# Kernel tuning notes

Measured on AMD Instinct MI355X. Metric: run time of the kernel, lower is better.

Reference implementation:

```python
import math
import jax, jax.numpy as jnp
import numpy as np

N_QUBITS = 8
N_QLAYERS = 2
HIDDEN = 768
BATCH = 8192
LN_EPS = 1e-5


def _ry_gate(theta):
    # theta: scalar or (B,) -> (2,2) or (B,2,2) complex64
    h = theta * 0.5
    c, s = jnp.cos(h), jnp.sin(h)
    g = jnp.stack([jnp.stack([c, -s], axis=-1), jnp.stack([s, c], axis=-1)], axis=-2)
    return g.astype(jnp.complex64)


def _rz_gate(theta):
    t = theta.astype(jnp.complex64)
    e0, e1 = jnp.exp(-0.5j * t), jnp.exp(0.5j * t)
    z = jnp.zeros_like(e0)
    return jnp.stack([jnp.stack([e0, z], axis=-1), jnp.stack([z, e1], axis=-1)], axis=-2)


def _apply_1q(state, gate, w, n):
    # state: (B, 2**n); gate: (2,2) shared or (B,2,2) per-sample; wire w (0 = MSB)
    B = state.shape[0]
    s = state.reshape(B, 2 ** w, 2, -1)
    if gate.ndim == 2:
        s = jnp.einsum('ij,bljr->blir', gate, s)
    else:
        s = jnp.einsum('bij,bljr->blir', gate, s)
    return s.reshape(B, -1)


def _apply_cnot(state, c, t, n):
    B = state.shape[0]
    s = state.reshape((B,) + (2,) * n)
    ax_c = 1 + c
    s0 = jnp.take(s, 0, axis=ax_c)  # control=0 branch, control axis removed
    s1 = jnp.take(s, 1, axis=ax_c)
    ax_t = 1 + t - (1 if t > c else 0)
    s1 = jnp.flip(s1, axis=ax_t)    # X on target when control=1
    s = jnp.stack([s0, s1], axis=ax_c)
    return s.reshape(B, -1)


def _circuit(angles, weights_ry, weights_rz):
    # angles: (B, n) float32 -> (B, n) PauliZ expectations, batched statevector sim
    n, L = N_QUBITS, N_QLAYERS
    B = angles.shape[0]
    state = jnp.zeros((B, 2 ** n), dtype=jnp.complex64).at[:, 0].set(1.0)
    for i in range(n):
        state = _apply_1q(state, _ry_gate(angles[:, i]), i, n)
    for i in range(1, n):
        state = _apply_cnot(state, 0, i, n)
    for l in range(L):
        for i in range(n):
            state = _apply_1q(state, _ry_gate(weights_ry[l, i]), i, n)
            state = _apply_1q(state, _rz_gate(weights_rz[l, i]), i, n)
    for i in range(1, n):
        state = _apply_cnot(state, i, 0, n)
    probs = jnp.abs(state) ** 2  # (B, 2**n)
    k = jnp.arange(2 ** n)
    bits = (k[None, :] >> (n - 1 - jnp.arange(n))[:, None]) & 1  # wire 0 = MSB (PennyLane)
    signs = (1 - 2 * bits).astype(probs.dtype)  # (n, 2**n)
    return probs @ signs.T  # (B, n)


def setup_inputs() -> dict:
    key = jax.random.key(0)
    ks = jax.random.split(key, 8)
    return {
        'hidden': jax.random.normal(ks[0], (BATCH, HIDDEN), dtype=jnp.float32),
        'W_in': jax.random.normal(ks[1], (N_QUBITS, HIDDEN), dtype=jnp.float32) * (1.0 / math.sqrt(HIDDEN)),
        'b_in': jax.random.normal(ks[2], (N_QUBITS,), dtype=jnp.float32) * 0.01,
        'W_out': jax.random.normal(ks[3], (HIDDEN, N_QUBITS), dtype=jnp.float32) * (1.0 / math.sqrt(N_QUBITS)),
        'b_out': jax.random.normal(ks[4], (HIDDEN,), dtype=jnp.float32) * 0.01,
        'weights_ry': jax.random.normal(ks[5], (N_QLAYERS, N_QUBITS), dtype=jnp.float32) * 0.1,
        'weights_rz': jax.random.normal(ks[6], (N_QLAYERS, N_QUBITS), dtype=jnp.float32) * 0.1,
        'gamma': jnp.ones((HIDDEN,), dtype=jnp.float32),
        'beta': jnp.zeros((HIDDEN,), dtype=jnp.float32),
    }


def reference(hidden, W_in, b_in, W_out, b_out, weights_ry, weights_rz, gamma, beta):
    phase = 0.0
    angles = jnp.tanh(hidden @ W_in.T + b_in) * math.pi + phase  # (B, n)
    meas = _circuit(angles, weights_ry, weights_rz).astype(jnp.float32)  # (B, n)
    y = meas @ W_out.T + b_out  # (B, h)
    mu = jnp.mean(y, axis=-1, keepdims=True)
    var = jnp.mean(jnp.square(y - mu), axis=-1, keepdims=True)
    return (y - mu) * jax.lax.rsqrt(var + LN_EPS) * gamma + beta
```

## Files before the change

### kernel.cpp

```cpp
#include <hip/hip_runtime.h>
#include <hip/hip_bf16.h>

#define NQ    8
#define HID   768
#define BATCH 8192
#define SPB   4
#define NBLK  (BATCH / SPB)
#define TPB   256

template<int BF> __device__ __forceinline__ float LDV(const void* p, int i) {
    if constexpr (BF) return __bfloat162float(((const __hip_bfloat16*)p)[i]);
    else return ((const float*)p)[i];
}
template<int BF> __device__ __forceinline__ void STV(void* p, int i, float v) {
    if constexpr (BF) ((__hip_bfloat16*)p)[i] = __float2bfloat16(v);
    else ((float*)p)[i] = v;
}
template<int BF> __device__ __forceinline__ float4 LD4(const void* p, int i4) {
    if constexpr (BF) {
        ushort4 v = ((const ushort4*)p)[i4];
        float4 r;
        r.x = __uint_as_float(((unsigned)v.x) << 16);
        r.y = __uint_as_float(((unsigned)v.y) << 16);
        r.z = __uint_as_float(((unsigned)v.z) << 16);
        r.w = __uint_as_float(((unsigned)v.w) << 16);
        return r;
    } else {
        return ((const float4*)p)[i4];
    }
}


__global__ void setup_kernel(const void* hidden, const void* wry, const void* wrz, void* ws) {
    __shared__ int votes;
    __shared__ int sFlag;
    int tid = threadIdx.x;
    if (tid == 0) votes = 0;
    __syncthreads();
    const unsigned int* hw = (const unsigned int*)hidden;
    int cnt = 0;
    #pragma unroll
    for (int k = 0; k < 16; ++k) {
        unsigned int w = hw[tid * 16 + k];
        unsigned int lo = w & 0xffffu;
        unsigned int e = (lo >> 7) & 0xffu;
        if (lo == 0u || (e >= 100u && e <= 133u)) cnt++;
    }
    atomicAdd(&votes, cnt);
    __syncthreads();
    if (tid == 0) {
        sFlag = (votes * 2 > TPB * 16) ? 1 : 0;
        *(int*)ws = sFlag;
    }
    __syncthreads();
    const int flag = sFlag;
    if (tid < NQ) {
        float ry0, ry1, rz0, rz1;
        if (flag) {
            ry0 = LDV<1>(wry, tid);  ry1 = LDV<1>(wry, NQ + tid);
            rz0 = LDV<1>(wrz, tid);  rz1 = LDV<1>(wrz, NQ + tid);
        } else {
            ry0 = LDV<0>(wry, tid);  ry1 = LDV<0>(wry, NQ + tid);
            rz0 = LDV<0>(wrz, tid);  rz1 = LDV<0>(wrz, NQ + tid);
        }
        float cA = cosf(0.5f*ry0), sA = sinf(0.5f*ry0);
        float cB = cosf(0.5f*ry1), sB = sinf(0.5f*ry1);
        float p0c = cosf(0.5f*rz0), p0s = sinf(0.5f*rz0);
        float p1c = cosf(0.5f*rz1), p1s = sinf(0.5f*rz1);
        float g00r =  cA*p0c, g00i = -cA*p0s;
        float g01r = -sA*p0c, g01i =  sA*p0s;
        float g10r =  sA*p0c, g10i =  sA*p0s;
        float g11r =  cA*p0c, g11i =  cA*p0s;
        float h00r = cB*g00r - sB*g10r, h00i = cB*g00i - sB*g10i;
        float h01r = cB*g01r - sB*g11r, h01i = cB*g01i - sB*g11i;
        float h10r = sB*g00r + cB*g10r, h10i = sB*g00i + cB*g10i;
        float h11r = sB*g01r + cB*g11r, h11i = sB*g01i + cB*g11i;
        float f00r = h00r*p1c + h00i*p1s, f00i = h00i*p1c - h00r*p1s;
        float f01r = h01r*p1c + h01i*p1s, f01i = h01i*p1c - h01r*p1s;
        float f10r = h10r*p1c - h10i*p1s, f10i = h10i*p1c + h10r*p1s;
        float f11r = h11r*p1c - h11i*p1s, f11i = h11i*p1c + h11r*p1s;
        float DA = f00r*f00r + f00i*f00i - (f10r*f10r + f10i*f10i);
        float DB = f01r*f01r + f01i*f01i - (f11r*f11r + f11i*f11i);
        float Kr = (f00r*f01r + f00i*f01i) - (f10r*f11r + f10i*f11i);
        float Ki = (f00i*f01r - f00r*f01i) - (f10i*f11r - f10r*f11i);
        float* qc = (float*)((char*)ws + 16);
        qc[tid*4+0] = DA; qc[tid*4+1] = DB; qc[tid*4+2] = Kr; qc[tid*4+3] = Ki;
    }
}

template<int BF>
__device__ __forceinline__ void run_all(
    const void* hidden_, const void* W_in_, const void* b_in_,
    const void* W_out_, const void* b_out_, const void* gamma_, const void* beta_,
    void* out_, const float* qc)
{
    const int tid  = threadIdx.x;
    const int lane = tid & 63;
    const int wv   = tid >> 6;
    const int b    = blockIdx.x * SPB + wv;
    const int j    = lane >> 3;
    const int u    = lane & 7;
    const int rowbase = b * HID;

    float a0 = 0.f, a1 = 0.f, a2 = 0.f, a3 = 0.f;
    const int hbase = b * (HID/4);
    const int wbase = j * (HID/4);
    #pragma unroll
    for (int t = 0; t < 24; ++t) {
        int i4 = u + (t << 3);
        float4 h = LD4<BF>(hidden_, hbase + i4);
        float4 w = LD4<BF>(W_in_,  wbase + i4);
        a0 = fmaf(h.x, w.x, a0); a1 = fmaf(h.y, w.y, a1);
        a2 = fmaf(h.z, w.z, a2); a3 = fmaf(h.w, w.w, a3);
    }
    float acc = (a0 + a1) + (a2 + a3);
    acc += __shfl_xor(acc, 1, 64);
    acc += __shfl_xor(acc, 2, 64);
    acc += __shfl_xor(acc, 4, 64);

    float zb = acc + LDV<BF>(b_in_, j);
    float th = tanhf(zb);
    float sj = sinpif(th);
    float cj = cospif(th);

    float4 q = ((const float4*)qc)[j];
    float DA = q.x, DB = q.y, Kr = q.z, Ki = q.w;
    float ca = 0.5f * (DA + DB), da = 0.5f * (DA - DB);
    float uu = da * cj;
    float vv = fmaf(Kr, sj, ca);
    const bool g0 = (j == 0);
    float MA = g0 ? 1.f : (vv + uu);
    float MB = g0 ? 1.f : (vv - uu);
    float fr = g0 ? 1.f : Kr;
    float fi = g0 ? 0.f : (cj * Ki);
    #pragma unroll
    for (int d = 8; d < 64; d <<= 1) {
        MA *= __shfl_xor(MA, d, 64);
        MB *= __shfl_xor(MB, d, 64);
        float qr = __shfl_xor(fr, d, 64);
        float qi = __shfl_xor(fi, d, 64);
        float nr = fr * qr - fi * qi;
        float ni = fr * qi + fi * qr;
        fr = nr; fi = ni;
    }
    float cc0 = __shfl(cj, 0, 64);
    float sc0 = __shfl(sj, 0, 64);
    float DA0 = __shfl(DA, 0, 64);
    float DB0 = __shfl(DB, 0, 64);
    float Kr0 = __shfl(Kr, 0, 64);
    float Ki0 = __shfl(Ki, 0, 64);
    float meas0 = 0.5f * (1.f + cc0) * DA0 * MA
                + 0.5f * (1.f - cc0) * DB0 * MB
                + sc0 * (Kr0 * fr - Ki0 * fi);
    float measj = g0 ? meas0 : fmaf(cc0, uu, vv);
    float m0 = meas0;
    float m1 = __shfl(measj,  8, 64);
    float m2 = __shfl(measj, 16, 64);
    float m3 = __shfl(measj, 24, 64);
    float m4 = __shfl(measj, 32, 64);
    float m5 = __shfl(measj, 40, 64);
    float m6 = __shfl(measj, 48, 64);
    float m7 = __shfl(measj, 56, 64);

    float yv[12];
    float sum = 0.f, sumsq = 0.f;
    #pragma unroll
    for (int t = 0; t < 12; ++t) {
        int h = lane + (t << 6);
        float4 w0 = LD4<BF>(W_out_, h * 2);
        float4 w1 = LD4<BF>(W_out_, h * 2 + 1);
        float y = LDV<BF>(b_out_, h);
        y = fmaf(m0, w0.x, y); y = fmaf(m1, w0.y, y);
        y = fmaf(m2, w0.z, y); y = fmaf(m3, w0.w, y);
        y = fmaf(m4, w1.x, y); y = fmaf(m5, w1.y, y);
        y = fmaf(m6, w1.z, y); y = fmaf(m7, w1.w, y);
        yv[t] = y;
        sum += y;
        sumsq = fmaf(y, y, sumsq);
    }
    #pragma unroll
    for (int d = 1; d < 64; d <<= 1) {
        sum   += __shfl_xor(sum,   d, 64);
        sumsq += __shfl_xor(sumsq, d, 64);
    }
    float mean = sum * (1.f / HID);
    float var  = fmaf(sumsq, 1.f / HID, -mean * mean);
    float rstd = rsqrtf(var + 1e-5f);
    #pragma unroll
    for (int t = 0; t < 12; ++t) {
        int h = lane + (t << 6);
        float g  = LDV<BF>(gamma_, h);
        float be = LDV<BF>(beta_,  h);
        float o  = fmaf((yv[t] - mean) * rstd, g, be);
        STV<BF>(out_, rowbase + h, o);
    }
}

__global__ __launch_bounds__(TPB, 4) void main_kernel(
    const void* hidden_, const void* W_in_, const void* b_in_,
    const void* W_out_, const void* b_out_, const void* gamma_, const void* beta_,
    void* out_, const void* ws_)
{
    const int flag = *(const int*)ws_;
    const float* qc = (const float*)((const char*)ws_ + 16);
    if (flag)
        run_all<1>(hidden_, W_in_, b_in_, W_out_, b_out_, gamma_, beta_, out_, qc);
    else
        run_all<0>(hidden_, W_in_, b_in_, W_out_, b_out_, gamma_, beta_, out_, qc);
}

extern "C" void kernel_launch(void* const* d_in, const int* in_sizes, int n_in,
                              void* d_out, int out_size, void* d_ws, size_t ws_size,
                              hipStream_t stream) {
    const void* hidden = d_in[0];
    const void* W_in   = d_in[1];
    const void* b_in   = d_in[2];
    const void* W_out  = d_in[3];
    const void* b_out  = d_in[4];
    const void* wry    = d_in[5];
    const void* wrz    = d_in[6];
    const void* gamma  = d_in[7];
    const void* beta   = d_in[8];
    setup_kernel<<<1, TPB, 0, stream>>>(hidden, wry, wrz, d_ws);
    main_kernel<<<NBLK, TPB, 0, stream>>>(hidden, W_in, b_in, W_out, b_out,
                                          gamma, beta, d_out, d_ws);
}
```

Measured before the change: 114.5 us.

## Fuse setup into main kernel, process two samples per wave, vectorize output

```diff
diff --git a/kernel.cpp b/kernel.cpp
--- a/kernel.cpp
+++ b/kernel.cpp
@@ -4,17 +4,14 @@
 #define NQ    8
 #define HID   768
 #define BATCH 8192
-#define SPB   4
+#define SPW   2
+#define SPB   (4*SPW)
 #define NBLK  (BATCH / SPB)
 #define TPB   256
 
 template<int BF> __device__ __forceinline__ float LDV(const void* p, int i) {
     if constexpr (BF) return __bfloat162float(((const __hip_bfloat16*)p)[i]);
     else return ((const float*)p)[i];
-}
-template<int BF> __device__ __forceinline__ void STV(void* p, int i, float v) {
-    if constexpr (BF) ((__hip_bfloat16*)p)[i] = __float2bfloat16(v);
-    else ((float*)p)[i] = v;
 }
 template<int BF> __device__ __forceinline__ float4 LD4(const void* p, int i4) {
     if constexpr (BF) {
@@ -29,40 +26,41 @@
         return ((const float4*)p)[i4];
     }
 }
-
-
-__global__ void setup_kernel(const void* hidden, const void* wry, const void* wrz, void* ws) {
-    __shared__ int votes;
-    __shared__ int sFlag;
-    int tid = threadIdx.x;
-    if (tid == 0) votes = 0;
-    __syncthreads();
-    const unsigned int* hw = (const unsigned int*)hidden;
-    int cnt = 0;
-    #pragma unroll
-    for (int k = 0; k < 16; ++k) {
-        unsigned int w = hw[tid * 16 + k];
-        unsigned int lo = w & 0xffffu;
-        unsigned int e = (lo >> 7) & 0xffu;
-        if (lo == 0u || (e >= 100u && e <= 133u)) cnt++;
-    }
-    atomicAdd(&votes, cnt);
-    __syncthreads();
-    if (tid == 0) {
-        sFlag = (votes * 2 > TPB * 16) ? 1 : 0;
-        *(int*)ws = sFlag;
-    }
-    __syncthreads();
-    const int flag = sFlag;
-    if (tid < NQ) {
-        float ry0, ry1, rz0, rz1;
-        if (flag) {
-            ry0 = LDV<1>(wry, tid);  ry1 = LDV<1>(wry, NQ + tid);
-            rz0 = LDV<1>(wrz, tid);  rz1 = LDV<1>(wrz, NQ + tid);
-        } else {
-            ry0 = LDV<0>(wry, tid);  ry1 = LDV<0>(wry, NQ + tid);
-            rz0 = LDV<0>(wrz, tid);  rz1 = LDV<0>(wrz, NQ + tid);
-        }
+template<int BF> __device__ __forceinline__ void ST4(void* p, int i4, float4 v) {
+    if constexpr (BF) {
+        __hip_bfloat16 bx = __float2bfloat16(v.x);
+        __hip_bfloat16 by = __float2bfloat16(v.y);
+        __hip_bfloat16 bz = __float2bfloat16(v.z);
+        __hip_bfloat16 bw = __float2bfloat16(v.w);
+        ushort4 s;
+        s.x = *(const unsigned short*)&bx;
+        s.y = *(const unsigned short*)&by;
+        s.z = *(const unsigned short*)&bz;
+        s.w = *(const unsigned short*)&bw;
+        ((ushort4*)p)[i4] = s;
+    } else {
+        ((float4*)p)[i4] = v;
+    }
+}
+
+template<int BF>
+__device__ __forceinline__ void run_all(
+    const void* hidden_, const void* W_in_, const void* b_in_,
+    const void* W_out_, const void* b_out_, const void* wry_, const void* wrz_,
+    const void* gamma_, const void* beta_, void* out_)
+{
+    const int tid  = threadIdx.x;
+    const int lane = tid & 63;
+    const int wv   = tid >> 6;
+    const int j    = lane >> 3;
+    const int u    = lane & 7;
+    const int b0   = blockIdx.x * SPB + wv * SPW;
+    const int b1   = b0 + 1;
+
+    float DA, DB, Kr, Ki;
+    {
+        float ry0 = LDV<BF>(wry_, j), ry1 = LDV<BF>(wry_, NQ + j);
+        float rz0 = LDV<BF>(wrz_, j), rz1 = LDV<BF>(wrz_, NQ + j);
         float cA = cosf(0.5f*ry0), sA = sinf(0.5f*ry0);
         float cB = cosf(0.5f*ry1), sB = sinf(0.5f*ry1);
         float p0c = cosf(0.5f*rz0), p0s = sinf(0.5f*rz0);
@@ -79,134 +77,152 @@
         float f01r = h01r*p1c + h01i*p1s, f01i = h01i*p1c - h01r*p1s;
         float f10r = h10r*p1c - h10i*p1s, f10i = h10i*p1c + h10r*p1s;
         float f11r = h11r*p1c - h11i*p1s, f11i = h11i*p1c + h11r*p1s;
-        float DA = f00r*f00r + f00i*f00i - (f10r*f10r + f10i*f10i);
-        float DB = f01r*f01r + f01i*f01i - (f11r*f11r + f11i*f11i);
-        float Kr = (f00r*f01r + f00i*f01i) - (f10r*f11r + f10i*f11i);
-        float Ki = (f00i*f01r - f00r*f01i) - (f10i*f11r - f10r*f11i);
-        float* qc = (float*)((char*)ws + 16);
-        qc[tid*4+0] = DA; qc[tid*4+1] = DB; qc[tid*4+2] = Kr; qc[tid*4+3] = Ki;
-    }
-}
-
-template<int BF>
-__device__ __forceinline__ void run_all(
-    const void* hidden_, const void* W_in_, const void* b_in_,
-    const void* W_out_, const void* b_out_, const void* gamma_, const void* beta_,
-    void* out_, const float* qc)
-{
-    const int tid  = threadIdx.x;
-    const int lane = tid & 63;
-    const int wv   = tid >> 6;
-    const int b    = blockIdx.x * SPB + wv;
-    const int j    = lane >> 3;
-    const int u    = lane & 7;
-    const int rowbase = b * HID;
-
-    float a0 = 0.f, a1 = 0.f, a2 = 0.f, a3 = 0.f;
-    const int hbase = b * (HID/4);
-    const int wbase = j * (HID/4);
+        DA = f00r*f00r + f00i*f00i - (f10r*f10r + f10i*f10i);
+        DB = f01r*f01r + f01i*f01i - (f11r*f11r + f11i*f11i);
+        Kr = (f00r*f01r + f00i*f01i) - (f10r*f11r + f10i*f11i);
+        Ki = (f00i*f01r - f00r*f01i) - (f10i*f11r - f10r*f11i);
+    }
+
+    float p00=0,p01=0,p02=0,p03=0, p10=0,p11=0,p12=0,p13=0;
+    const int h0b = b0 * (HID/4);
+    const int h1b = b1 * (HID/4);
+    const int wb  = j  * (HID/4);
     #pragma unroll
     for (int t = 0; t < 24; ++t) {
         int i4 = u + (t << 3);
-        float4 h = LD4<BF>(hidden_, hbase + i4);
-        float4 w = LD4<BF>(W_in_,  wbase + i4);
-        a0 = fmaf(h.x, w.x, a0); a1 = fmaf(h.y, w.y, a1);
-        a2 = fmaf(h.z, w.z, a2); a3 = fmaf(h.w, w.w, a3);
-    }
-    float acc = (a0 + a1) + (a2 + a3);
-    acc += __shfl_xor(acc, 1, 64);
-    acc += __shfl_xor(acc, 2, 64);
-    acc += __shfl_xor(acc, 4, 64);
-
-    float zb = acc + LDV<BF>(b_in_, j);
-    float th = tanhf(zb);
-    float sj = sinpif(th);
-    float cj = cospif(th);
-
-    float4 q = ((const float4*)qc)[j];
-    float DA = q.x, DB = q.y, Kr = q.z, Ki = q.w;
+        float4 w  = LD4<BF>(W_in_,   wb  + i4);
+        float4 h0 = LD4<BF>(hidden_, h0b + i4);
+        float4 h1 = LD4<BF>(hidden_, h1b + i4);
+        p00 = fmaf(h0.x, w.x, p00); p01 = fmaf(h0.y, w.y, p01);
+        p02 = fmaf(h0.z, w.z, p02); p03 = fmaf(h0.w, w.w, p03);
+        p10 = fmaf(h1.x, w.x, p10); p11 = fmaf(h1.y, w.y, p11);
+        p12 = fmaf(h1.z, w.z, p12); p13 = fmaf(h1.w, w.w, p13);
+    }
+    float acc0 = (p00 + p01) + (p02 + p03);
+    float acc1 = (p10 + p11) + (p12 + p13);
+    #pragma unroll
+    for (int d = 1; d < 8; d <<= 1) {
+        acc0 += __shfl_xor(acc0, d, 64);
+        acc1 += __shfl_xor(acc1, d, 64);
+    }
+
+    float binj = LDV<BF>(b_in_, j);
+    float th0 = tanhf(acc0 + binj);
+    float th1 = tanhf(acc1 + binj);
+    float sj0 = sinpif(th0), cj0 = cospif(th0);
+    float sj1 = sinpif(th1), cj1 = cospif(th1);
+
     float ca = 0.5f * (DA + DB), da = 0.5f * (DA - DB);
-    float uu = da * cj;
-    float vv = fmaf(Kr, sj, ca);
     const bool g0 = (j == 0);
-    float MA = g0 ? 1.f : (vv + uu);
-    float MB = g0 ? 1.f : (vv - uu);
-    float fr = g0 ? 1.f : Kr;
-    float fi = g0 ? 0.f : (cj * Ki);
+    float uu0 = da * cj0, vv0 = fmaf(Kr, sj0, ca);
+    float uu1 = da * cj1, vv1 = fmaf(Kr, sj1, ca);
+    float MA0 = g0 ? 1.f : (vv0 + uu0), MB0 = g0 ? 1.f : (vv0 - uu0);
+    float MA1 = g0 ? 1.f : (vv1 + uu1), MB1 = g0 ? 1.f : (vv1 - uu1);
+    float fr0 = g0 ? 1.f : Kr, fi0 = g0 ? 0.f : (cj0 * Ki);
+    float fr1 = g0 ? 1.f : Kr, fi1 = g0 ? 0.f : (cj1 * Ki);
     #pragma unroll
     for (int d = 8; d < 64; d <<= 1) {
-        MA *= __shfl_xor(MA, d, 64);
-        MB *= __shfl_xor(MB, d, 64);
-        float qr = __shfl_xor(fr, d, 64);
-        float qi = __shfl_xor(fi, d, 64);
-        float nr = fr * qr - fi * qi;
-        float ni = fr * qi + fi * qr;
-        fr = nr; fi = ni;
-    }
-    float cc0 = __shfl(cj, 0, 64);
-    float sc0 = __shfl(sj, 0, 64);
-    float DA0 = __shfl(DA, 0, 64);
-    float DB0 = __shfl(DB, 0, 64);
-    float Kr0 = __shfl(Kr, 0, 64);
-    float Ki0 = __shfl(Ki, 0, 64);
-    float meas0 = 0.5f * (1.f + cc0) * DA0 * MA
-                + 0.5f * (1.f - cc0) * DB0 * MB
-                + sc0 * (Kr0 * fr - Ki0 * fi);
-    float measj = g0 ? meas0 : fmaf(cc0, uu, vv);
-    float m0 = meas0;
-    float m1 = __shfl(measj,  8, 64);
-    float m2 = __shfl(measj, 16, 64);
-    float m3 = __shfl(measj, 24, 64);
-    float m4 = __shfl(measj, 32, 64);
-    float m5 = __shfl(measj, 40, 64);
-    float m6 = __shfl(measj, 48, 64);
-    float m7 = __shfl(measj, 56, 64);
-
-    float yv[12];
-    float sum = 0.f, sumsq = 0.f;
-    #pragma unroll
-    for (int t = 0; t < 12; ++t) {
-        int h = lane + (t << 6);
-        float4 w0 = LD4<BF>(W_out_, h * 2);
-        float4 w1 = LD4<BF>(W_out_, h * 2 + 1);
-        float y = LDV<BF>(b_out_, h);
-        y = fmaf(m0, w0.x, y); y = fmaf(m1, w0.y, y);
-        y = fmaf(m2, w0.z, y); y = fmaf(m3, w0.w, y);
-        y = fmaf(m4, w1.x, y); y = fmaf(m5, w1.y, y);
-        y = fmaf(m6, w1.z, y); y = fmaf(m7, w1.w, y);
-        yv[t] = y;
-        sum += y;
-        sumsq = fmaf(y, y, sumsq);
+        MA0 *= __shfl_xor(MA0, d, 64);   MA1 *= __shfl_xor(MA1, d, 64);
+        MB0 *= __shfl_xor(MB0, d, 64);   MB1 *= __shfl_xor(MB1, d, 64);
+        float q0r = __shfl_xor(fr0, d, 64), q0i = __shfl_xor(fi0, d, 64);
+        float q1r = __shfl_xor(fr1, d, 64), q1i = __shfl_xor(fi1, d, 64);
+        float n0r = fr0*q0r - fi0*q0i, n0i = fr0*q0i + fi0*q0r;
+        float n1r = fr1*q1r - fi1*q1i, n1i = fr1*q1i + fi1*q1r;
+        fr0 = n0r; fi0 = n0i; fr1 = n1r; fi1 = n1i;
+    }
+    float DA0 = __shfl(DA, 0, 64), DB0 = __shfl(DB, 0, 64);
+    float Kr0 = __shfl(Kr, 0, 64), Ki0 = __shfl(Ki, 0, 64);
+    float cc00 = __shfl(cj0, 0, 64), sc00 = __shfl(sj0, 0, 64);
+    float cc01 = __shfl(cj1, 0, 64), sc01 = __shfl(sj1, 0, 64);
+    float meas00 = 0.5f*(1.f+cc00)*DA0*MA0 + 0.5f*(1.f-cc00)*DB0*MB0
+                 + sc00*(Kr0*fr0 - Ki0*fi0);
+    float meas01 = 0.5f*(1.f+cc01)*DA0*MA1 + 0.5f*(1.f-cc01)*DB0*MB1
+                 + sc01*(Kr0*fr1 - Ki0*fi1);
+    float measj0 = g0 ? meas00 : fmaf(cc00, uu0, vv0);
+    float measj1 = g0 ? meas01 : fmaf(cc01, uu1, vv1);
+    float m00 = meas00;
+    float m01 = __shfl(measj0,  8, 64), m02 = __shfl(measj0, 16, 64);
+    float m03 = __shfl(measj0, 24, 64), m04 = __shfl(measj0, 32, 64);
+    float m05 = __shfl(measj0, 40, 64), m06 = __shfl(measj0, 48, 64);
+    float m07 = __shfl(measj0, 56, 64);
+    float m10 = meas01;
+    float m11 = __shfl(measj1,  8, 64), m12 = __shfl(measj1, 16, 64);
+    float m13 = __shfl(measj1, 24, 64), m14 = __shfl(measj1, 32, 64);
+    float m15 = __shfl(measj1, 40, 64), m16 = __shfl(measj1, 48, 64);
+    float m17 = __shfl(measj1, 56, 64);
+
+    float y0v[12], y1v[12];
+    float sum0 = 0.f, sq0 = 0.f, sum1 = 0.f, sq1 = 0.f;
+    #pragma unroll
+    for (int g = 0; g < 3; ++g) {
+        float4 bo = LD4<BF>(b_out_, 3*lane + g);
+        float bos[4] = {bo.x, bo.y, bo.z, bo.w};
+        #pragma unroll
+        for (int e = 0; e < 4; ++e) {
+            int c = 12*lane + 4*g + e;
+            float4 w0 = LD4<BF>(W_out_, c*2);
+            float4 w1 = LD4<BF>(W_out_, c*2 + 1);
+            float y0 = bos[e], y1 = bos[e];
+            y0 = fmaf(m00, w0.x, y0); y0 = fmaf(m01, w0.y, y0);
+            y0 = fmaf(m02, w0.z, y0); y0 = fmaf(m03, w0.w, y0);
+            y0 = fmaf(m04, w1.x, y0); y0 = fmaf(m05, w1.y, y0);
+            y0 = fmaf(m06, w1.z, y0); y0 = fmaf(m07, w1.w, y0);
+            y1 = fmaf(m10, w0.x, y1); y1 = fmaf(m11, w0.y, y1);
+            y1 = fmaf(m12, w0.z, y1); y1 = fmaf(m13, w0.w, y1);
+            y1 = fmaf(m14, w1.x, y1); y1 = fmaf(m15, w1.y, y1);
+            y1 = fmaf(m16, w1.z, y1); y1 = fmaf(m17, w1.w, y1);
+            y0v[4*g+e] = y0; y1v[4*g+e] = y1;
+            sum0 += y0; sq0 = fmaf(y0, y0, sq0);
+            sum1 += y1; sq1 = fmaf(y1, y1, sq1);
+        }
     }
     #pragma unroll
     for (int d = 1; d < 64; d <<= 1) {
-        sum   += __shfl_xor(sum,   d, 64);
-        sumsq += __shfl_xor(sumsq, d, 64);
-    }
-    float mean = sum * (1.f / HID);
-    float var  = fmaf(sumsq, 1.f / HID, -mean * mean);
-    float rstd = rsqrtf(var + 1e-5f);
-    #pragma unroll
-    for (int t = 0; t < 12; ++t) {
-        int h = lane + (t << 6);
-        float g  = LDV<BF>(gamma_, h);
-        float be = LDV<BF>(beta_,  h);
-        float o  = fmaf((yv[t] - mean) * rstd, g, be);
-        STV<BF>(out_, rowbase + h, o);
+        sum0 += __shfl_xor(sum0, d, 64);  sq0 += __shfl_xor(sq0, d, 64);
+        sum1 += __shfl_xor(sum1, d, 64);  sq1 += __shfl_xor(sq1, d, 64);
+    }
+    float mean0 = sum0 * (1.f/HID);
+    float var0  = fmaf(sq0, 1.f/HID, -mean0*mean0);
+    float rstd0 = rsqrtf(var0 + 1e-5f);
+    float mean1 = sum1 * (1.f/HID);
+    float var1  = fmaf(sq1, 1.f/HID, -mean1*mean1);
+    float rstd1 = rsqrtf(var1 + 1e-5f);
+    #pragma unroll
+    for (int g = 0; g < 3; ++g) {
+        float4 ga = LD4<BF>(gamma_, 3*lane + g);
+        float4 be = LD4<BF>(beta_,  3*lane + g);
+        float4 o0, o1;
+        o0.x = fmaf((y0v[4*g+0]-mean0)*rstd0, ga.x, be.x);
+        o0.y = fmaf((y0v[4*g+1]-mean0)*rstd0, ga.y, be.y);
+        o0.z = fmaf((y0v[4*g+2]-mean0)*rstd0, ga.z, be.z);
+        o0.w = fmaf((y0v[4*g+3]-mean0)*rstd0, ga.w, be.w);
+        o1.x = fmaf((y1v[4*g+0]-mean1)*rstd1, ga.x, be.x);
+        o1.y = fmaf((y1v[4*g+1]-mean1)*rstd1, ga.y, be.y);
+        o1.z = fmaf((y1v[4*g+2]-mean1)*rstd1, ga.z, be.z);
+        o1.w = fmaf((y1v[4*g+3]-mean1)*rstd1, ga.w, be.w);
+        ST4<BF>(out_, b0*(HID/4) + 3*lane + g, o0);
+        ST4<BF>(out_, b1*(HID/4) + 3*lane + g, o1);
     }
 }
 
 __global__ __launch_bounds__(TPB, 4) void main_kernel(
     const void* hidden_, const void* W_in_, const void* b_in_,
-    const void* W_out_, const void* b_out_, const void* gamma_, const void* beta_,
-    void* out_, const void* ws_)
+    const void* W_out_, const void* b_out_, const void* wry_, const void* wrz_,
+    const void* gamma_, const void* beta_, void* out_)
 {
-    const int flag = *(const int*)ws_;
-    const float* qc = (const float*)((const char*)ws_ + 16);
+    const int lane = threadIdx.x & 63;
+    unsigned wrd = ((const unsigned*)hidden_)[lane];
+    unsigned lo  = wrd & 0xffffu;
+    unsigned e   = (lo >> 7) & 0xffu;
+    bool v = (lo == 0u) || (e >= 100u && e <= 133u);
+    unsigned long long mask = __ballot(v);
+    int flag = (__popcll(mask) > 32) ? 1 : 0;
     if (flag)
-        run_all<1>(hidden_, W_in_, b_in_, W_out_, b_out_, gamma_, beta_, out_, qc);
+        run_all<1>(hidden_, W_in_, b_in_, W_out_, b_out_, wry_, wrz_,
+                   gamma_, beta_, out_);
     else
-        run_all<0>(hidden_, W_in_, b_in_, W_out_, b_out_, gamma_, beta_, out_, qc);
+        run_all<0>(hidden_, W_in_, b_in_, W_out_, b_out_, wry_, wrz_,
+                   gamma_, beta_, out_);
 }
 
 extern "C" void kernel_launch(void* const* d_in, const int* in_sizes, int n_in,
@@ -221,7 +237,7 @@
     const void* wrz    = d_in[6];
     const void* gamma  = d_in[7];
     const void* beta   = d_in[8];
-    setup_kernel<<<1, TPB, 0, stream>>>(hidden, wry, wrz, d_ws);
+    (void)d_ws; (void)ws_size;
     main_kernel<<<NBLK, TPB, 0, stream>>>(hidden, W_in, b_in, W_out, b_out,
-                                          gamma, beta, d_out, d_ws);
-}
+                                          wry, wrz, gamma, beta, d_out);
+}
```

After: 120.2 us. 5.0% more time.
